# Performance work log

Hardware: AMD Instinct MI355X
Metric: run time of the kernel (lower is better)

## Reference

```python
import jax, jax.numpy as jnp
import numpy as np

B, Q, K, D = 32, 2048, 2048, 128
MASK_VAL = -1000000.0


def setup_inputs() -> dict:
    key = jax.random.key(0)
    kq, kk, kv, km = jax.random.split(key, 4)
    queries = jax.random.normal(kq, (B, Q, D), dtype=jnp.float32)
    keys = jax.random.normal(kk, (B, K, D), dtype=jnp.float32)
    values = jax.random.normal(kv, (B, K, D), dtype=jnp.float32)
    mask_idx = jax.random.randint(km, (B, Q, K), 0, 2).astype(jnp.bool_)
    return {"queries": queries, "keys": keys, "values": values, "mask_idx": mask_idx}


def reference(queries, keys, values, mask_idx):
    d = queries.shape[-1]
    # scores: [B, Q, K]
    scores = jnp.einsum('bqd,bkd->bqk', queries, keys) / jnp.sqrt(jnp.asarray(d, queries.dtype))
    # scores[mask_idx] = -1e6 (boolean assignment -> where)
    scores = jnp.where(mask_idx, jnp.asarray(MASK_VAL, scores.dtype), scores)
    attn = jax.nn.softmax(scores, axis=-1)
    # dropout p=0.0 (eval / deterministic reference) -> identity
    return jnp.einsum('bqk,bkv->bqv', attn, values)
```

## Files before the change

kernel.cpp:

```cpp
#include <hip/hip_runtime.h>

typedef __attribute__((ext_vector_type(8))) short bf16x8;
typedef __attribute__((ext_vector_type(4))) short s16x4;
typedef __attribute__((ext_vector_type(16))) float f32x16;

#define LOG2E 1.4426950408889634f
#define MASKV2 (-1442695.0f)
#define GAS __attribute__((address_space(1)))
#define LAS __attribute__((address_space(3)))

__device__ __forceinline__ unsigned cvt_pk_bf16(float lo, float hi_) {
  unsigned r;
  asm("v_cvt_pk_bf16_f32 %0, %1, %2" : "=v"(r) : "v"(lo), "v"(hi_));
  return r;
}

__global__ void detect_mask_kernel(const unsigned char* __restrict__ m, int* flag) {
  __shared__ unsigned s[64];
  const int tid = threadIdx.x;
  unsigned acc = 0;
  const uint4* p = (const uint4*)m;
#pragma unroll
  for (int i = 0; i < 16; ++i) {
    uint4 a = p[tid + i * 256];
    acc |= (a.x | a.y | a.z | a.w) & 0xFFFFFF00u;
  }
  acc = acc | (unsigned)__shfl_xor((int)acc, 1);
  acc = acc | (unsigned)__shfl_xor((int)acc, 2);
  acc = acc | (unsigned)__shfl_xor((int)acc, 4);
  acc = acc | (unsigned)__shfl_xor((int)acc, 8);
  acc = acc | (unsigned)__shfl_xor((int)acc, 16);
  acc = acc | (unsigned)__shfl_xor((int)acc, 32);
  if ((tid & 63) == 0) s[tid >> 6] = acc;
  __syncthreads();
  if (tid == 0) flag[0] = ((s[0] | s[1] | s[2] | s[3]) != 0) ? 1 : 0;
}

__global__ __launch_bounds__(512)
void build_images(const float* __restrict__ Kp, const float* __restrict__ Vp,
                  char* __restrict__ img)
{
  const int tid  = threadIdx.x;
  const int tile = blockIdx.x;
  const int b = tile >> 5, kt = tile & 31;
  __shared__ __align__(16) short Kl[64 * 128];
  __shared__ __align__(16) short Vt[128 * 64];
  const size_t kvbase = ((size_t)b * 2048 + (size_t)kt * 64) * 128;

  const int krow0 = tid >> 5, kcol0 = (tid & 31) * 4;
#pragma unroll
  for (int i = 0; i < 4; ++i) {
    const int row = krow0 + i * 16;
    float4 x = *(const float4*)(Kp + kvbase + row * 128 + kcol0);
    union { s16x4 v; unsigned u[2]; } pk;
    pk.u[0] = cvt_pk_bf16(x.x, x.y);
    pk.u[1] = cvt_pk_bf16(x.z, x.w);
    *(s16x4*)&Kl[row * 128 + (kcol0 ^ (8 * (row & 15)))] = pk.v;
  }
  {
    const int db = tid & 31, kb = tid >> 5;
    union { float4 v; float f[4]; } r0, r1, r2, r3;
    r0.v = *(const float4*)(Vp + kvbase + (kb * 4 + 0) * 128 + db * 4);
    r1.v = *(const float4*)(Vp + kvbase + (kb * 4 + 1) * 128 + db * 4);
    r2.v = *(const float4*)(Vp + kvbase + (kb * 4 + 2) * 128 + db * 4);
    r3.v = *(const float4*)(Vp + kvbase + (kb * 4 + 3) * 128 + db * 4);
    const int cs = (kb * 4) ^ (8 * (db & 7));
#pragma unroll
    for (int j = 0; j < 4; ++j) {
      union { s16x4 v; unsigned u[2]; } pk;
      pk.u[0] = cvt_pk_bf16(r0.f[j], r1.f[j]);
      pk.u[1] = cvt_pk_bf16(r2.f[j], r3.f[j]);
      *(s16x4*)&Vt[(db * 4 + j) * 64 + cs] = pk.v;
    }
  }
  __syncthreads();
  char* o = img + (size_t)tile * 32768;
  *(uint4*)(o +     0 + tid * 16) = *(const uint4*)((const char*)Kl +    0 + tid * 16);
  *(uint4*)(o +  8192 + tid * 16) = *(const uint4*)((const char*)Kl + 8192 + tid * 16);
  *(uint4*)(o + 16384 + tid * 16) = *(const uint4*)((const char*)Vt +    0 + tid * 16);
  *(uint4*)(o + 24576 + tid * 16) = *(const uint4*)((const char*)Vt + 8192 + tid * 16);
}

__global__ __launch_bounds__(256, 2)
void attn13(const float* __restrict__ Qp, const unsigned char* __restrict__ M8,
            const char* __restrict__ img, float* __restrict__ Op,
            const int* __restrict__ flag)
{
  const int tid  = threadIdx.x;
  const int lane = tid & 63;
  const int wv   = tid >> 6;
  const int hi   = lane >> 5;
  const int l31  = lane & 31;
  const int n    = blockIdx.x;
  const int b    = (n & 7) + 8 * (n >> 7);
  const int qt   = (n >> 3) & 15;
  const int q    = qt * 128 + wv * 32 + l31;
  const bool is8 = (flag[0] != 0);

  __shared__ __align__(16) short Kl[2][64 * 128];
  __shared__ __align__(16) short Vt[2][128 * 64];

  const float qscale = 0.08838834764831845f * LOG2E;
  bf16x8 qf[8];
  {
    const float* qrow = Qp + ((size_t)b * 2048 + q) * 128;
#pragma unroll
    for (int dc = 0; dc < 8; ++dc) {
      const int d0 = dc * 16 + hi * 8;
      float4 x = *(const float4*)(qrow + d0);
      float4 y = *(const float4*)(qrow + d0 + 4);
      union { bf16x8 v; unsigned u[4]; } uu;
      uu.u[0] = cvt_pk_bf16(x.x * qscale, x.y * qscale);
      uu.u[1] = cvt_pk_bf16(x.z * qscale, x.w * qscale);
      uu.u[2] = cvt_pk_bf16(y.x * qscale, y.y * qscale);
      uu.u[3] = cvt_pk_bf16(y.z * qscale, y.w * qscale);
      qf[dc] = uu.v;
    }
  }

  f32x16 oacc[4];
#pragma unroll
  for (int gg = 0; gg < 4; ++gg)
#pragma unroll
    for (int r = 0; r < 16; ++r) oacc[gg][r] = 0.f;

  float mrun = -1e30f, lrun = 0.f;
  const unsigned char* mrow8  = M8 + ((size_t)b * 2048 + q) * (size_t)2048;
  const int*           mrow32 = (const int*)M8 + ((size_t)b * 2048 + q) * (size_t)2048;
  const int xk = 8 * (l31 & 15);
  const int xv = 8 * (l31 >> 2);
  const char* imgb = img + (size_t)(b * 32) * 32768;
  const int wb4 = wv * 4096;

#define DMA_TILE13(t_, slot_)                                                                   \
  do {                                                                                           \
    const char* s_ = imgb + (size_t)(t_) * 32768;                                                \
    char* kd_ = (char*)&Kl[slot_][0] + wb4;                                                      \
    char* vd_ = (char*)&Vt[slot_][0] + wb4;                                                      \
    _Pragma("unroll")                                                                            \
    for (int j_ = 0; j_ < 4; ++j_) {                                                             \
      __builtin_amdgcn_global_load_lds((const GAS unsigned*)(s_ + wb4 + j_ * 1024 + lane * 16),  \
                                       (LAS unsigned*)(kd_ + j_ * 1024), 16, 0, 0);              \
      __builtin_amdgcn_global_load_lds((const GAS unsigned*)(s_ + 16384 + wb4 + j_ * 1024 + lane * 16), \
                                       (LAS unsigned*)(vd_ + j_ * 1024), 16, 0, 0);              \
    }                                                                                            \
  } while (0)

  DMA_TILE13(0, 0);
  __syncthreads();

  for (int kt = 0; kt < 32; ++kt) {
    const int cur = kt & 1;
    const short* klb = &Kl[cur][0];
    const short* vtb = &Vt[cur][0];

    if (kt < 31) DMA_TILE13(kt + 1, cur ^ 1);

    unsigned mg[8];
    if (is8) {
#pragma unroll
      for (int m = 0; m < 4; ++m) {
        mg[m]     = *(const unsigned*)(mrow8 + kt * 64 + hi * 4 + m * 8);
        mg[4 + m] = *(const unsigned*)(mrow8 + kt * 64 + 32 + hi * 4 + m * 8);
      }
    }

    f32x16 s0m, s1m;
#pragma unroll
    for (int r = 0; r < 16; ++r) { s0m[r] = 0.f; s1m[r] = 0.f; }
    __builtin_amdgcn_s_setprio(1);
#pragma unroll
    for (int dc = 0; dc < 8; ++dc) {
      const int colb = (dc * 16 + hi * 8) ^ xk;
      bf16x8 a0 = *(const bf16x8*)&klb[l31 * 128 + colb];
      bf16x8 a1 = *(const bf16x8*)&klb[(32 + l31) * 128 + colb];
      s0m = __builtin_amdgcn_mfma_f32_32x32x16_bf16(a0, qf[dc], s0m, 0, 0, 0);
      s1m = __builtin_amdgcn_mfma_f32_32x32x16_bf16(a1, qf[dc], s1m, 0, 0, 0);
    }
    __builtin_amdgcn_s_setprio(0);

    if (is8) {
#pragma unroll
      for (int m = 0; m < 4; ++m)
#pragma unroll
        for (int e = 0; e < 4; ++e) {
          s0m[4 * m + e] = ((mg[m]     >> (8 * e)) & 0xffu) ? MASKV2 : s0m[4 * m + e];
          s1m[4 * m + e] = ((mg[4 + m] >> (8 * e)) & 0xffu) ? MASKV2 : s1m[4 * m + e];
        }
    } else {
#pragma unroll
      for (int m = 0; m < 4; ++m) {
        int4 w0 = *(const int4*)(mrow32 + kt * 64 + hi * 4 + m * 8);
        int4 w1 = *(const int4*)(mrow32 + kt * 64 + 32 + hi * 4 + m * 8);
        s0m[4 * m + 0] = w0.x ? MASKV2 : s0m[4 * m + 0];
        s0m[4 * m + 1] = w0.y ? MASKV2 : s0m[4 * m + 1];
        s0m[4 * m + 2] = w0.z ? MASKV2 : s0m[4 * m + 2];
        s0m[4 * m + 3] = w0.w ? MASKV2 : s0m[4 * m + 3];
        s1m[4 * m + 0] = w1.x ? MASKV2 : s1m[4 * m + 0];
        s1m[4 * m + 1] = w1.y ? MASKV2 : s1m[4 * m + 1];
        s1m[4 * m + 2] = w1.z ? MASKV2 : s1m[4 * m + 2];
        s1m[4 * m + 3] = w1.w ? MASKV2 : s1m[4 * m + 3];
      }
    }

    float v[16];
#pragma unroll
    for (int r = 0; r < 16; ++r) v[r] = fmaxf(s0m[r], s1m[r]);
#pragma unroll
    for (int st = 8; st > 0; st >>= 1)
#pragma unroll
      for (int r = 0; r < 8; ++r)
        if (r < st) v[r] = fmaxf(v[r], v[r + st]);
    float tm = fmaxf(v[0], __shfl_xor(v[0], 32));

    if (__any(tm > mrun + 8.0f)) {
      float mnew = fmaxf(mrun, tm);
      float corr = __builtin_amdgcn_exp2f(mrun - mnew);
      mrun = mnew; lrun *= corr;
#pragma unroll
      for (int gg = 0; gg < 4; ++gg)
#pragma unroll
        for (int r = 0; r < 16; ++r) oacc[gg][r] *= corr;
    }

#pragma unroll
    for (int r = 0; r < 16; ++r) s0m[r] = __builtin_amdgcn_exp2f(s0m[r] - mrun);
#pragma unroll
    for (int r = 0; r < 16; ++r) s1m[r] = __builtin_amdgcn_exp2f(s1m[r] - mrun);
    float w[16];
#pragma unroll
    for (int r = 0; r < 16; ++r) w[r] = s0m[r] + s1m[r];
#pragma unroll
    for (int st = 8; st > 0; st >>= 1)
#pragma unroll
      for (int r = 0; r < 8; ++r)
        if (r < st) w[r] += w[r + st];
    lrun += w[0] + __shfl_xor(w[0], 32);

    unsigned pk0[8], pk1[8];
#pragma unroll
    for (int i = 0; i < 8; ++i) {
      pk0[i] = cvt_pk_bf16(s0m[2 * i], s0m[2 * i + 1]);
      pk1[i] = cvt_pk_bf16(s1m[2 * i], s1m[2 * i + 1]);
    }
    bf16x8 pa[4];
#pragma unroll
    for (int ks = 0; ks < 4; ++ks) {
      const int base = 4 * (ks & 1);
      unsigned o0, o1, sd0, sd1;
      if (ks < 2) {
        o0  = hi ? pk0[base + 2] : pk0[base + 0];
        o1  = hi ? pk0[base + 3] : pk0[base + 1];
        sd0 = hi ? pk0[base + 0] : pk0[base + 2];
        sd1 = hi ? pk0[base + 1] : pk0[base + 3];
      } else {
        o0  = hi ? pk1[base + 2] : pk1[base + 0];
        o1  = hi ? pk1[base + 3] : pk1[base + 1];
        sd0 = hi ? pk1[base + 0] : pk1[base + 2];
        sd1 = hi ? pk1[base + 1] : pk1[base + 3];
      }
      unsigned rec0 = (unsigned)__shfl_xor((int)sd0, 32);
      unsigned rec1 = (unsigned)__shfl_xor((int)sd1, 32);
      union { bf16x8 v; unsigned u[4]; } uu;
      uu.u[0] = hi ? rec0 : o0;
      uu.u[1] = hi ? rec1 : o1;
      uu.u[2] = hi ? o0 : rec0;
      uu.u[3] = hi ? o1 : rec1;
      pa[ks] = uu.v;
    }

    __builtin_amdgcn_s_setprio(1);
#pragma unroll
    for (int gg = 0; gg < 4; ++gg) {
      const int drow = gg * 32 + l31;
#pragma unroll
      for (int ks = 0; ks < 4; ++ks) {
        bf16x8 va = *(const bf16x8*)&vtb[drow * 64 + ((ks * 16 + hi * 8) ^ xv)];
        oacc[gg] = __builtin_amdgcn_mfma_f32_32x32x16_bf16(va, pa[ks], oacc[gg], 0, 0, 0);
      }
    }
    __builtin_amdgcn_s_setprio(0);

    __syncthreads();
  }
#undef DMA_TILE13

  const float inv = 1.0f / lrun;
  float* orow = Op + ((size_t)b * 2048 + q) * 128;
#pragma unroll
  for (int gg = 0; gg < 4; ++gg) {
#pragma unroll
    for (int m = 0; m < 4; ++m) {
      float4 o;
      o.x = oacc[gg][4 * m + 0] * inv;
      o.y = oacc[gg][4 * m + 1] * inv;
      o.z = oacc[gg][4 * m + 2] * inv;
      o.w = oacc[gg][4 * m + 3] * inv;
      *(float4*)(orow + gg * 32 + hi * 4 + m * 8) = o;
    }
  }
}

__global__ __launch_bounds__(512, 2)
void attn_fb(const float* __restrict__ Qp, const float* __restrict__ Kp,
             const float* __restrict__ Vp, const unsigned char* __restrict__ M8,
             float* __restrict__ Op, const int* __restrict__ flag)
{
  const int tid  = threadIdx.x;
  const int lane = tid & 63;
  const int wv   = tid >> 6;
  const int hi   = lane >> 5;
  const int l31  = lane & 31;
  const int n    = blockIdx.x;
  const int b    = (n & 7) + 8 * (n >> 6);
  const int qt   = (n >> 3) & 7;
  const int q    = qt * 256 + wv * 32 + l31;
  const bool is8 = (flag[0] != 0);

  __shared__ __align__(16) short Kl[2][64 * 128];
  __shared__ __align__(16) short Vt[2][128 * 64];

  const float qscale = 0.08838834764831845f * LOG2E;
  bf16x8 qf[8];
  {
    const float* qrow = Qp + ((size_t)b * 2048 + q) * 128;
#pragma unroll
    for (int dc = 0; dc < 8; ++dc) {
      const int d0 = dc * 16 + hi * 8;
      float4 x = *(const float4*)(qrow + d0);
      float4 y = *(const float4*)(qrow + d0 + 4);
      union { bf16x8 v; unsigned u[4]; } uu;
      uu.u[0] = cvt_pk_bf16(x.x * qscale, x.y * qscale);
      uu.u[1] = cvt_pk_bf16(x.z * qscale, x.w * qscale);
      uu.u[2] = cvt_pk_bf16(y.x * qscale, y.y * qscale);
      uu.u[3] = cvt_pk_bf16(y.z * qscale, y.w * qscale);
      qf[dc] = uu.v;
    }
  }
  f32x16 oacc[4];
#pragma unroll
  for (int gg = 0; gg < 4; ++gg)
#pragma unroll
    for (int r = 0; r < 16; ++r) oacc[gg][r] = 0.f;
  float mrun = -1e30f, lrun = 0.f;
  const unsigned char* mrow8  = M8 + ((size_t)b * 2048 + q) * (size_t)2048;
  const int*           mrow32 = (const int*)M8 + ((size_t)b * 2048 + q) * (size_t)2048;
  const int xk = 8 * (l31 & 15);
  const int xv = 8 * (l31 >> 2);
  const int db = tid & 31, kb = tid >> 5;
  const size_t kvrow0 = (size_t)b * 2048 * 128;
  const int krow0 = tid >> 5, kcol0 = (tid & 31) * 4;

  {
#pragma unroll
    for (int i = 0; i < 4; ++i) {
      const int row = krow0 + i * 16;
      float4 x = *(const float4*)(Kp + kvrow0 + row * 128 + kcol0);
      union { s16x4 v; unsigned u[2]; } pk;
      pk.u[0] = cvt_pk_bf16(x.x, x.y);
      pk.u[1] = cvt_pk_bf16(x.z, x.w);
      *(s16x4*)&Kl[0][row * 128 + (kcol0 ^ (8 * (row & 15)))] = pk.v;
    }
    union { float4 v; float f[4]; } r0, r1, r2, r3;
    r0.v = *(const float4*)(Vp + kvrow0 + (kb * 4 + 0) * 128 + db * 4);
    r1.v = *(const float4*)(Vp + kvrow0 + (kb * 4 + 1) * 128 + db * 4);
    r2.v = *(const float4*)(Vp + kvrow0 + (kb * 4 + 2) * 128 + db * 4);
    r3.v = *(const float4*)(Vp + kvrow0 + (kb * 4 + 3) * 128 + db * 4);
    const int cs = (kb * 4) ^ (8 * (db & 7));
#pragma unroll
    for (int j = 0; j < 4; ++j) {
      union { s16x4 v; unsigned u[2]; } pk;
      pk.u[0] = cvt_pk_bf16(r0.f[j], r1.f[j]);
      pk.u[1] = cvt_pk_bf16(r2.f[j], r3.f[j]);
      *(s16x4*)&Vt[0][(db * 4 + j) * 64 + cs] = pk.v;
    }
  }
  __syncthreads();

  for (int kt = 0; kt < 32; ++kt) {
    const int cur = kt & 1;
    const short* klb = &Kl[cur][0];
    const short* vtb = &Vt[cur][0];
    const int ktn = (kt < 31) ? kt + 1 : 31;
    const size_t nb = kvrow0 + (size_t)ktn * 64 * 128;
    float4 kreg[4], vreg[4];
#pragma unroll
    for (int i = 0; i < 4; ++i)
      kreg[i] = *(const float4*)(Kp + nb + (krow0 + i * 16) * 128 + kcol0);
#pragma unroll
    for (int i = 0; i < 4; ++i)
      vreg[i] = *(const float4*)(Vp + nb + (kb * 4 + i) * 128 + db * 4);

    f32x16 s0m, s1m;
#pragma unroll
    for (int r = 0; r < 16; ++r) { s0m[r] = 0.f; s1m[r] = 0.f; }
#pragma unroll
    for (int dc = 0; dc < 8; ++dc) {
      const int colb = (dc * 16 + hi * 8) ^ xk;
      bf16x8 a0 = *(const bf16x8*)&klb[l31 * 128 + colb];
      bf16x8 a1 = *(const bf16x8*)&klb[(32 + l31) * 128 + colb];
      s0m = __builtin_amdgcn_mfma_f32_32x32x16_bf16(a0, qf[dc], s0m, 0, 0, 0);
      s1m = __builtin_amdgcn_mfma_f32_32x32x16_bf16(a1, qf[dc], s1m, 0, 0, 0);
    }
    if (is8) {
#pragma unroll
      for (int m = 0; m < 4; ++m) {
        unsigned w0 = *(const unsigned*)(mrow8 + kt * 64 + hi * 4 + m * 8);
        unsigned w1 = *(const unsigned*)(mrow8 + kt * 64 + 32 + hi * 4 + m * 8);
#pragma unroll
        for (int e = 0; e < 4; ++e) {
          s0m[4 * m + e] = ((w0 >> (8 * e)) & 0xffu) ? MASKV2 : s0m[4 * m + e];
          s1m[4 * m + e] = ((w1 >> (8 * e)) & 0xffu) ? MASKV2 : s1m[4 * m + e];
        }
      }
    } else {
#pragma unroll
      for (int m = 0; m < 4; ++m) {
        int4 w0 = *(const int4*)(mrow32 + kt * 64 + hi * 4 + m * 8);
        int4 w1 = *(const int4*)(mrow32 + kt * 64 + 32 + hi * 4 + m * 8);
        s0m[4 * m + 0] = w0.x ? MASKV2 : s0m[4 * m + 0];
        s0m[4 * m + 1] = w0.y ? MASKV2 : s0m[4 * m + 1];
        s0m[4 * m + 2] = w0.z ? MASKV2 : s0m[4 * m + 2];
        s0m[4 * m + 3] = w0.w ? MASKV2 : s0m[4 * m + 3];
        s1m[4 * m + 0] = w1.x ? MASKV2 : s1m[4 * m + 0];
        s1m[4 * m + 1] = w1.y ? MASKV2 : s1m[4 * m + 1];
        s1m[4 * m + 2] = w1.z ? MASKV2 : s1m[4 * m + 2];
        s1m[4 * m + 3] = w1.w ? MASKV2 : s1m[4 * m + 3];
      }
    }
    float tm = s0m[0];
#pragma unroll
    for (int r = 1; r < 16; ++r) tm = fmaxf(tm, s0m[r]);
#pragma unroll
    for (int r = 0; r < 16; ++r) tm = fmaxf(tm, s1m[r]);
    tm = fmaxf(tm, __shfl_xor(tm, 32));
    if (__any(tm > mrun + 8.0f)) {
      float mnew = fmaxf(mrun, tm);
      float corr = __builtin_amdgcn_exp2f(mrun - mnew);
      mrun = mnew; lrun *= corr;
#pragma unroll
      for (int gg = 0; gg < 4; ++gg)
#pragma unroll
        for (int r = 0; r < 16; ++r) oacc[gg][r] *= corr;
    }
    float psum = 0.f;
#pragma unroll
    for (int r = 0; r < 16; ++r) { s0m[r] = __builtin_amdgcn_exp2f(s0m[r] - mrun); psum += s0m[r]; }
#pragma unroll
    for (int r = 0; r < 16; ++r) { s1m[r] = __builtin_amdgcn_exp2f(s1m[r] - mrun); psum += s1m[r]; }
    psum += __shfl_xor(psum, 32);
    lrun += psum;
    unsigned pk0[8], pk1[8];
#pragma unroll
    for (int i = 0; i < 8; ++i) {
      pk0[i] = cvt_pk_bf16(s0m[2 * i], s0m[2 * i + 1]);
      pk1[i] = cvt_pk_bf16(s1m[2 * i], s1m[2 * i + 1]);
    }
    bf16x8 pa[4];
#pragma unroll
    for (int ks = 0; ks < 4; ++ks) {
      const int base = 4 * (ks & 1);
      unsigned o0, o1, sd0, sd1;
      if (ks < 2) {
        o0  = hi ? pk0[base + 2] : pk0[base + 0];
        o1  = hi ? pk0[base + 3] : pk0[base + 1];
        sd0 = hi ? pk0[base + 0] : pk0[base + 2];
        sd1 = hi ? pk0[base + 1] : pk0[base + 3];
      } else {
        o0  = hi ? pk1[base + 2] : pk1[base + 0];
        o1  = hi ? pk1[base + 3] : pk1[base + 1];
        sd0 = hi ? pk1[base + 0] : pk1[base + 2];
        sd1 = hi ? pk1[base + 1] : pk1[base + 3];
      }
      unsigned rec0 = (unsigned)__shfl_xor((int)sd0, 32);
      unsigned rec1 = (unsigned)__shfl_xor((int)sd1, 32);
      union { bf16x8 v; unsigned u[4]; } uu;
      uu.u[0] = hi ? rec0 : o0;
      uu.u[1] = hi ? rec1 : o1;
      uu.u[2] = hi ? o0 : rec0;
      uu.u[3] = hi ? o1 : rec1;
      pa[ks] = uu.v;
    }
#pragma unroll
    for (int gg = 0; gg < 4; ++gg) {
      const int drow = gg * 32 + l31;
#pragma unroll
      for (int ks = 0; ks < 4; ++ks) {
        bf16x8 va = *(const bf16x8*)&vtb[drow * 64 + ((ks * 16 + hi * 8) ^ xv)];
        oacc[gg] = __builtin_amdgcn_mfma_f32_32x32x16_bf16(va, pa[ks], oacc[gg], 0, 0, 0);
      }
    }
    {
      short* kln = &Kl[cur ^ 1][0];
      short* vtn = &Vt[cur ^ 1][0];
#pragma unroll
      for (int i = 0; i < 4; ++i) {
        const int row = krow0 + i * 16;
        union { s16x4 v; unsigned u[2]; } pk;
        pk.u[0] = cvt_pk_bf16(kreg[i].x, kreg[i].y);
        pk.u[1] = cvt_pk_bf16(kreg[i].z, kreg[i].w);
        *(s16x4*)&kln[row * 128 + (kcol0 ^ (8 * (row & 15)))] = pk.v;
      }
      const int cs = (kb * 4) ^ (8 * (db & 7));
#pragma unroll
      for (int j = 0; j < 4; ++j) {
        union { s16x4 v; unsigned u[2]; } pk;
        union { float4 v; float f[4]; } a0, a1, a2, a3;
        a0.v = vreg[0]; a1.v = vreg[1]; a2.v = vreg[2]; a3.v = vreg[3];
        pk.u[0] = cvt_pk_bf16(a0.f[j], a1.f[j]);
        pk.u[1] = cvt_pk_bf16(a2.f[j], a3.f[j]);
        *(s16x4*)&vtn[(db * 4 + j) * 64 + cs] = pk.v;
      }
    }
    __syncthreads();
  }
  const float inv = 1.0f / lrun;
  float* orow = Op + ((size_t)b * 2048 + q) * 128;
#pragma unroll
  for (int gg = 0; gg < 4; ++gg) {
#pragma unroll
    for (int m = 0; m < 4; ++m) {
      float4 o;
      o.x = oacc[gg][4 * m + 0] * inv;
      o.y = oacc[gg][4 * m + 1] * inv;
      o.z = oacc[gg][4 * m + 2] * inv;
      o.w = oacc[gg][4 * m + 3] * inv;
      *(float4*)(orow + gg * 32 + hi * 4 + m * 8) = o;
    }
  }
}

extern "C" void kernel_launch(void* const* d_in, const int* in_sizes, int n_in,
                              void* d_out, int out_size, void* d_ws, size_t ws_size,
                              hipStream_t stream) {
  const float* qp = (const float*)d_in[0];
  const float* kp = (const float*)d_in[1];
  const float* vp = (const float*)d_in[2];
  const unsigned char* mp = (const unsigned char*)d_in[3];
  float* op = (float*)d_out;
  int* flag = (int*)d_ws;

  detect_mask_kernel<<<1, 256, 0, stream>>>(mp, flag);

  const size_t need = 256 + (size_t)1024 * 32768;
  if (ws_size >= need) {
    char* img = (char*)d_ws + 256;
    build_images<<<1024, 512, 0, stream>>>(kp, vp, img);
    attn13<<<512, 256, 0, stream>>>(qp, mp, img, op, flag);
  } else {
    attn_fb<<<256, 512, 0, stream>>>(qp, kp, vp, mp, op, flag);
  }
}
```

Measured before the change: 202.9 us.

## Shrink attention blocks to two waves and drop LDS double buffering

The kernel now runs 1024 blocks of 128 threads, each covering 64 queries instead of 128, and uses a single LDS K/V tile instead of a double-buffered pair. One wave loads the K half and the other the V half, and the next tile is fetched synchronously after each iteration. The goal is lower LDS use per block and more resident blocks per CU, so that overlap comes from other blocks rather than in-block prefetch. The trade-off is exposed load latency within each block, twice as many reads of the K/V image per query, and an extra barrier per iteration.

```diff
diff --git a/kernel.cpp b/kernel.cpp
--- a/kernel.cpp
+++ b/kernel.cpp
@@ -81,8 +81,8 @@
   *(uint4*)(o + 24576 + tid * 16) = *(const uint4*)((const char*)Vt + 8192 + tid * 16);
 }
 
-__global__ __launch_bounds__(256, 2)
-void attn13(const float* __restrict__ Qp, const unsigned char* __restrict__ M8,
+__global__ __launch_bounds__(128)
+void attn14(const float* __restrict__ Qp, const unsigned char* __restrict__ M8,
             const char* __restrict__ img, float* __restrict__ Op,
             const int* __restrict__ flag)
 {
@@ -92,13 +92,13 @@
   const int hi   = lane >> 5;
   const int l31  = lane & 31;
   const int n    = blockIdx.x;
-  const int b    = (n & 7) + 8 * (n >> 7);
-  const int qt   = (n >> 3) & 15;
-  const int q    = qt * 128 + wv * 32 + l31;
+  const int b    = (n & 7) + 8 * (n >> 8);
+  const int qt   = (n >> 3) & 31;
+  const int q    = qt * 64 + wv * 32 + l31;
   const bool is8 = (flag[0] != 0);
 
-  __shared__ __align__(16) short Kl[2][64 * 128];
-  __shared__ __align__(16) short Vt[2][128 * 64];
+  __shared__ __align__(16) short Kl[64 * 128];
+  __shared__ __align__(16) short Vt[128 * 64];
 
   const float qscale = 0.08838834764831845f * LOG2E;
   bf16x8 qf[8];
@@ -130,32 +130,23 @@
   const int xk = 8 * (l31 & 15);
   const int xv = 8 * (l31 >> 2);
   const char* imgb = img + (size_t)(b * 32) * 32768;
-  const int wb4 = wv * 4096;
-
-#define DMA_TILE13(t_, slot_)                                                                   \
-  do {                                                                                           \
-    const char* s_ = imgb + (size_t)(t_) * 32768;                                                \
-    char* kd_ = (char*)&Kl[slot_][0] + wb4;                                                      \
-    char* vd_ = (char*)&Vt[slot_][0] + wb4;                                                      \
-    _Pragma("unroll")                                                                            \
-    for (int j_ = 0; j_ < 4; ++j_) {                                                             \
-      __builtin_amdgcn_global_load_lds((const GAS unsigned*)(s_ + wb4 + j_ * 1024 + lane * 16),  \
-                                       (LAS unsigned*)(kd_ + j_ * 1024), 16, 0, 0);              \
-      __builtin_amdgcn_global_load_lds((const GAS unsigned*)(s_ + 16384 + wb4 + j_ * 1024 + lane * 16), \
-                                       (LAS unsigned*)(vd_ + j_ * 1024), 16, 0, 0);              \
-    }                                                                                            \
+
+  char* const dseg = wv ? (char*)&Vt[0] : (char*)&Kl[0];
+  const int  soff  = wv * 16384;
+
+#define DMA14(t_)                                                                       \
+  do {                                                                                   \
+    const char* s_ = imgb + (size_t)(t_) * 32768 + soff;                                 \
+    _Pragma("unroll")                                                                    \
+    for (int j_ = 0; j_ < 16; ++j_)                                                      \
+      __builtin_amdgcn_global_load_lds((const GAS unsigned*)(s_ + j_ * 1024 + lane * 16),\
+                                       (LAS unsigned*)(dseg + j_ * 1024), 16, 0, 0);     \
   } while (0)
 
-  DMA_TILE13(0, 0);
+  DMA14(0);
   __syncthreads();
 
   for (int kt = 0; kt < 32; ++kt) {
-    const int cur = kt & 1;
-    const short* klb = &Kl[cur][0];
-    const short* vtb = &Vt[cur][0];
-
-    if (kt < 31) DMA_TILE13(kt + 1, cur ^ 1);
-
     unsigned mg[8];
     if (is8) {
 #pragma unroll
@@ -172,8 +163,8 @@
 #pragma unroll
     for (int dc = 0; dc < 8; ++dc) {
       const int colb = (dc * 16 + hi * 8) ^ xk;
-      bf16x8 a0 = *(const bf16x8*)&klb[l31 * 128 + colb];
-      bf16x8 a1 = *(const bf16x8*)&klb[(32 + l31) * 128 + colb];
+      bf16x8 a0 = *(const bf16x8*)&Kl[l31 * 128 + colb];
+      bf16x8 a1 = *(const bf16x8*)&Kl[(32 + l31) * 128 + colb];
       s0m = __builtin_amdgcn_mfma_f32_32x32x16_bf16(a0, qf[dc], s0m, 0, 0, 0);
       s1m = __builtin_amdgcn_mfma_f32_32x32x16_bf16(a1, qf[dc], s1m, 0, 0, 0);
     }
@@ -275,15 +266,19 @@
       const int drow = gg * 32 + l31;
 #pragma unroll
       for (int ks = 0; ks < 4; ++ks) {
-        bf16x8 va = *(const bf16x8*)&vtb[drow * 64 + ((ks * 16 + hi * 8) ^ xv)];
+        bf16x8 va = *(const bf16x8*)&Vt[drow * 64 + ((ks * 16 + hi * 8) ^ xv)];
         oacc[gg] = __builtin_amdgcn_mfma_f32_32x32x16_bf16(va, pa[ks], oacc[gg], 0, 0, 0);
       }
     }
     __builtin_amdgcn_s_setprio(0);
 
     __syncthreads();
-  }
-#undef DMA_TILE13
+    if (kt < 31) {
+      DMA14(kt + 1);
+      __syncthreads();
+    }
+  }
+#undef DMA14
 
   const float inv = 1.0f / lrun;
   float* orow = Op + ((size_t)b * 2048 + q) * 128;
@@ -546,7 +541,7 @@
   if (ws_size >= need) {
     char* img = (char*)d_ws + 256;
     build_images<<<1024, 512, 0, stream>>>(kp, vp, img);
-    attn13<<<512, 256, 0, stream>>>(qp, mp, img, op, flag);
+    attn14<<<1024, 128, 0, stream>>>(qp, mp, img, op, flag);
   } else {
     attn_fb<<<256, 512, 0, stream>>>(qp, kp, vp, mp, op, flag);
   }
```

New measurement: 276.9 us. +36.4%, slower.

## Software-pipeline QK^T one tile ahead of softmax and PV

Applied to the files above, without the earlier changes.

Restructures the attention main loop so the QK^T MFMAs for tile kt+1 are issued before the softmax and PV work of tile kt, with the K tile prefetched two steps ahead and V one step ahead in separate DMA streams. The aim is to overlap the matrix units with the exp/max/convert VALU work in the same wave. The cost is an extra 32 accumulator registers for the second score buffer, which may hurt occupancy at two blocks per CU or cause spills.

```diff
diff --git a/kernel.cpp b/kernel.cpp
--- a/kernel.cpp
+++ b/kernel.cpp
@@ -82,7 +82,7 @@
 }
 
 __global__ __launch_bounds__(256, 2)
-void attn13(const float* __restrict__ Qp, const unsigned char* __restrict__ M8,
+void attn16(const float* __restrict__ Qp, const unsigned char* __restrict__ M8,
             const char* __restrict__ img, float* __restrict__ Op,
             const int* __restrict__ flag)
 {
@@ -132,29 +132,52 @@
   const char* imgb = img + (size_t)(b * 32) * 32768;
   const int wb4 = wv * 4096;
 
-#define DMA_TILE13(t_, slot_)                                                                   \
-  do {                                                                                           \
-    const char* s_ = imgb + (size_t)(t_) * 32768;                                                \
-    char* kd_ = (char*)&Kl[slot_][0] + wb4;                                                      \
-    char* vd_ = (char*)&Vt[slot_][0] + wb4;                                                      \
-    _Pragma("unroll")                                                                            \
-    for (int j_ = 0; j_ < 4; ++j_) {                                                             \
-      __builtin_amdgcn_global_load_lds((const GAS unsigned*)(s_ + wb4 + j_ * 1024 + lane * 16),  \
-                                       (LAS unsigned*)(kd_ + j_ * 1024), 16, 0, 0);              \
-      __builtin_amdgcn_global_load_lds((const GAS unsigned*)(s_ + 16384 + wb4 + j_ * 1024 + lane * 16), \
-                                       (LAS unsigned*)(vd_ + j_ * 1024), 16, 0, 0);              \
-    }                                                                                            \
+#define DMAK(t_, slot_)                                                                          \
+  do {                                                                                            \
+    const char* s_ = imgb + (size_t)(t_) * 32768 + wb4;                                           \
+    char* d_ = (char*)&Kl[slot_][0] + wb4;                                                        \
+    _Pragma("unroll")                                                                             \
+    for (int j_ = 0; j_ < 4; ++j_)                                                                \
+      __builtin_amdgcn_global_load_lds((const GAS unsigned*)(s_ + j_ * 1024 + lane * 16),         \
+                                       (LAS unsigned*)(d_ + j_ * 1024), 16, 0, 0);                \
   } while (0)
-
-  DMA_TILE13(0, 0);
+#define DMAV(t_, slot_)                                                                           \
+  do {                                                                                            \
+    const char* s_ = imgb + (size_t)(t_) * 32768 + 16384 + wb4;                                   \
+    char* d_ = (char*)&Vt[slot_][0] + wb4;                                                        \
+    _Pragma("unroll")                                                                             \
+    for (int j_ = 0; j_ < 4; ++j_)                                                                \
+      __builtin_amdgcn_global_load_lds((const GAS unsigned*)(s_ + j_ * 1024 + lane * 16),         \
+                                       (LAS unsigned*)(d_ + j_ * 1024), 16, 0, 0);                \
+  } while (0)
+
+#define QK16(slot_, s0_, s1_)                                                        \
+  do {                                                                                \
+    const short* klb_ = &Kl[slot_][0];                                                \
+    _Pragma("unroll")                                                                 \
+    for (int r = 0; r < 16; ++r) { (s0_)[r] = 0.f; (s1_)[r] = 0.f; }                  \
+    _Pragma("unroll")                                                                 \
+    for (int dc = 0; dc < 8; ++dc) {                                                  \
+      const int colb_ = (dc * 16 + hi * 8) ^ xk;                                      \
+      bf16x8 a0_ = *(const bf16x8*)&klb_[l31 * 128 + colb_];                          \
+      bf16x8 a1_ = *(const bf16x8*)&klb_[(32 + l31) * 128 + colb_];                   \
+      (s0_) = __builtin_amdgcn_mfma_f32_32x32x16_bf16(a0_, qf[dc], (s0_), 0, 0, 0);   \
+      (s1_) = __builtin_amdgcn_mfma_f32_32x32x16_bf16(a1_, qf[dc], (s1_), 0, 0, 0);   \
+    }                                                                                 \
+  } while (0)
+
+  DMAK(0, 0);
+  DMAV(0, 0);
+  DMAK(1, 1);
   __syncthreads();
 
+  f32x16 s0A, s1A, s0B, s1B;
+  QK16(0, s0A, s1A);
+  __syncthreads();
+
   for (int kt = 0; kt < 32; ++kt) {
-    const int cur = kt & 1;
-    const short* klb = &Kl[cur][0];
-    const short* vtb = &Vt[cur][0];
-
-    if (kt < 31) DMA_TILE13(kt + 1, cur ^ 1);
+    if (kt < 30) DMAK(kt + 2, kt & 1);
+    if (kt < 31) DMAV(kt + 1, (kt + 1) & 1);
 
     unsigned mg[8];
     if (is8) {
@@ -165,47 +188,39 @@
       }
     }
 
-    f32x16 s0m, s1m;
-#pragma unroll
-    for (int r = 0; r < 16; ++r) { s0m[r] = 0.f; s1m[r] = 0.f; }
-    __builtin_amdgcn_s_setprio(1);
-#pragma unroll
-    for (int dc = 0; dc < 8; ++dc) {
-      const int colb = (dc * 16 + hi * 8) ^ xk;
-      bf16x8 a0 = *(const bf16x8*)&klb[l31 * 128 + colb];
-      bf16x8 a1 = *(const bf16x8*)&klb[(32 + l31) * 128 + colb];
-      s0m = __builtin_amdgcn_mfma_f32_32x32x16_bf16(a0, qf[dc], s0m, 0, 0, 0);
-      s1m = __builtin_amdgcn_mfma_f32_32x32x16_bf16(a1, qf[dc], s1m, 0, 0, 0);
-    }
-    __builtin_amdgcn_s_setprio(0);
+    if (kt < 31) {
+      __builtin_amdgcn_s_setprio(1);
+      QK16((kt + 1) & 1, s0B, s1B);
+      __builtin_amdgcn_s_setprio(0);
+    }
 
     if (is8) {
 #pragma unroll
       for (int m = 0; m < 4; ++m)
 #pragma unroll
         for (int e = 0; e < 4; ++e) {
-          s0m[4 * m + e] = ((mg[m]     >> (8 * e)) & 0xffu) ? MASKV2 : s0m[4 * m + e];
-          s1m[4 * m + e] = ((mg[4 + m] >> (8 * e)) & 0xffu) ? MASKV2 : s1m[4 * m + e];
+          s0A[4 * m + e] = ((mg[m]     >> (8 * e)) & 0xffu) ? MASKV2 : s0A[4 * m + e];
+          s1A[4 * m + e] = ((mg[4 + m] >> (8 * e)) & 0xffu) ? MASKV2 : s1A[4 * m + e];
         }
     } else {
 #pragma unroll
       for (int m = 0; m < 4; ++m) {
         int4 w0 = *(const int4*)(mrow32 + kt * 64 + hi * 4 + m * 8);
         int4 w1 = *(const int4*)(mrow32 + kt * 64 + 32 + hi * 4 + m * 8);
-        s0m[4 * m + 0] = w0.x ? MASKV2 : s0m[4 * m + 0];
-        s0m[4 * m + 1] = w0.y ? MASKV2 : s0m[4 * m + 1];
-        s0m[4 * m + 2] = w0.z ? MASKV2 : s0m[4 * m + 2];
-        s0m[4 * m + 3] = w0.w ? MASKV2 : s0m[4 * m + 3];
-        s1m[4 * m + 0] = w1.x ? MASKV2 : s1m[4 * m + 0];
-        s1m[4 * m + 1] = w1.y ? MASKV2 : s1m[4 * m + 1];
-        s1m[4 * m + 2] = w1.z ? MASKV2 : s1m[4 * m + 2];
-        s1m[4 * m + 3] = w1.w ? MASKV2 : s1m[4 * m + 3];
+        s0A[4 * m + 0] = w0.x ? MASKV2 : s0A[4 * m + 0];
+        s0A[4 * m + 1] = w0.y ? MASKV2 : s0A[4 * m + 1];
+        s0A[4 * m + 2] = w0.z ? MASKV2 : s0A[4 * m + 2];
+        s0A[4 * m + 3] = w0.w ? MASKV2 : s0A[4 * m + 3];
+        s1A[4 * m + 0] = w1.x ? MASKV2 : s1A[4 * m + 0];
+        s1A[4 * m + 1] = w1.y ? MASKV2 : s1A[4 * m + 1];
+        s1A[4 * m + 2] = w1.z ? MASKV2 : s1A[4 * m + 2];
+        s1A[4 * m + 3] = w1.w ? MASKV2 : s1A[4 * m + 3];
       }
     }
 
     float v[16];
 #pragma unroll
-    for (int r = 0; r < 16; ++r) v[r] = fmaxf(s0m[r], s1m[r]);
+    for (int r = 0; r < 16; ++r) v[r] = fmaxf(s0A[r], s1A[r]);
 #pragma unroll
     for (int st = 8; st > 0; st >>= 1)
 #pragma unroll
@@ -224,12 +239,12 @@
     }
 
 #pragma unroll
-    for (int r = 0; r < 16; ++r) s0m[r] = __builtin_amdgcn_exp2f(s0m[r] - mrun);
-#pragma unroll
-    for (int r = 0; r < 16; ++r) s1m[r] = __builtin_amdgcn_exp2f(s1m[r] - mrun);
+    for (int r = 0; r < 16; ++r) s0A[r] = __builtin_amdgcn_exp2f(s0A[r] - mrun);
+#pragma unroll
+    for (int r = 0; r < 16; ++r) s1A[r] = __builtin_amdgcn_exp2f(s1A[r] - mrun);
     float w[16];
 #pragma unroll
-    for (int r = 0; r < 16; ++r) w[r] = s0m[r] + s1m[r];
+    for (int r = 0; r < 16; ++r) w[r] = s0A[r] + s1A[r];
 #pragma unroll
     for (int st = 8; st > 0; st >>= 1)
 #pragma unroll
@@ -240,8 +255,8 @@
     unsigned pk0[8], pk1[8];
 #pragma unroll
     for (int i = 0; i < 8; ++i) {
-      pk0[i] = cvt_pk_bf16(s0m[2 * i], s0m[2 * i + 1]);
-      pk1[i] = cvt_pk_bf16(s1m[2 * i], s1m[2 * i + 1]);
+      pk0[i] = cvt_pk_bf16(s0A[2 * i], s0A[2 * i + 1]);
+      pk1[i] = cvt_pk_bf16(s1A[2 * i], s1A[2 * i + 1]);
     }
     bf16x8 pa[4];
 #pragma unroll
@@ -269,21 +284,28 @@
       pa[ks] = uu.v;
     }
 
-    __builtin_amdgcn_s_setprio(1);
-#pragma unroll
-    for (int gg = 0; gg < 4; ++gg) {
-      const int drow = gg * 32 + l31;
-#pragma unroll
-      for (int ks = 0; ks < 4; ++ks) {
-        bf16x8 va = *(const bf16x8*)&vtb[drow * 64 + ((ks * 16 + hi * 8) ^ xv)];
-        oacc[gg] = __builtin_amdgcn_mfma_f32_32x32x16_bf16(va, pa[ks], oacc[gg], 0, 0, 0);
-      }
-    }
-    __builtin_amdgcn_s_setprio(0);
+    {
+      const short* vtb = &Vt[kt & 1][0];
+      __builtin_amdgcn_s_setprio(1);
+#pragma unroll
+      for (int gg = 0; gg < 4; ++gg) {
+        const int drow = gg * 32 + l31;
+#pragma unroll
+        for (int ks = 0; ks < 4; ++ks) {
+          bf16x8 va = *(const bf16x8*)&vtb[drow * 64 + ((ks * 16 + hi * 8) ^ xv)];
+          oacc[gg] = __builtin_amdgcn_mfma_f32_32x32x16_bf16(va, pa[ks], oacc[gg], 0, 0, 0);
+        }
+      }
+      __builtin_amdgcn_s_setprio(0);
+    }
+
+    if (kt < 31) { s0A = s0B; s1A = s1B; }
 
     __syncthreads();
   }
-#undef DMA_TILE13
+#undef DMAK
+#undef DMAV
+#undef QK16
 
   const float inv = 1.0f / lrun;
   float* orow = Op + ((size_t)b * 2048 + q) * 128;
@@ -546,7 +568,7 @@
   if (ws_size >= need) {
     char* img = (char*)d_ws + 256;
     build_images<<<1024, 512, 0, stream>>>(kp, vp, img);
-    attn13<<<512, 256, 0, stream>>>(qp, mp, img, op, flag);
+    attn16<<<512, 256, 0, stream>>>(qp, mp, img, op, flag);
   } else {
     attn_fb<<<256, 512, 0, stream>>>(qp, kp, vp, mp, op, flag);
   }
```

New measurement: 202.1 us. No clear change (-0.4%).
